# Optimization experiments

Measured on AMD Instinct MI355X. Metric: run time of the kernel, lower is better.

## Reference

```python
import jax, jax.numpy as jnp
import numpy as np

B = 8192      # sessions
L = 64        # tokens per session
T = B * L     # total tokens
H = 128       # hidden_size
MAX_LEN = 64  # position_emb has MAX_LEN+1 rows


def setup_inputs() -> dict:
    key = jax.random.key(0)
    ks = jax.random.split(key, 10)
    s1 = 1.0 / np.sqrt(H)
    s2 = 1.0 / np.sqrt(2 * H)
    hidden = jax.random.normal(ks[0], (T, H), jnp.float32)
    seq_len = jnp.full((B,), L, dtype=jnp.int32)
    # reversed positions 1..L within each session (<= MAX_LEN)
    reverse_pos = jnp.tile(jnp.arange(L, 0, -1, dtype=jnp.int32), B)
    return {
        "hidden": hidden,
        "pos_table": jax.random.normal(ks[1], (MAX_LEN + 1, H), jnp.float32) * 0.02,
        "W_pos_w": jax.random.normal(ks[2], (H, 2 * H), jnp.float32) * s2,
        "W_pos_b": jax.random.normal(ks[3], (H,), jnp.float32) * s2,
        "W1_w": jax.random.normal(ks[4], (H, H), jnp.float32) * s1,
        "W1_b": jax.random.normal(ks[5], (H,), jnp.float32) * s1,
        "W2_w": jax.random.normal(ks[6], (H, H), jnp.float32) * s1,
        "W2_b": jax.random.normal(ks[7], (H,), jnp.float32) * s1,
        "q_w": jax.random.normal(ks[8], (1, H), jnp.float32) * s1,
        "q_b": jax.random.normal(ks[9], (1,), jnp.float32) * s1,
        "seq_len": seq_len,
        "reverse_pos": reverse_pos,
    }


def reference(hidden, pos_table, W_pos_w, W_pos_b, W1_w, W1_b, W2_w, W2_b,
              q_w, q_b, seq_len, reverse_pos):
    Bn = seq_len.shape[0]
    Tn = hidden.shape[0]
    # token -> session id (replaces the python split loop)
    seg = jnp.repeat(jnp.arange(Bn), seq_len, total_repeat_length=Tn)  # [T]
    # per-session mean, broadcast back to tokens (v_mean_repeat_concat)
    mean = jax.ops.segment_sum(hidden, seg, num_segments=Bn) \
        / seq_len[:, None].astype(hidden.dtype)                        # [B,H]
    mean_rep = mean[seg]                                               # [T,H]
    pos_emb = pos_table[reverse_pos]                                   # [T,H]
    pos_hidden = jnp.tanh(
        jnp.concatenate([hidden, pos_emb], axis=-1) @ W_pos_w.T + W_pos_b
    )                                                                  # [T,H]
    gate = jax.nn.sigmoid(mean_rep @ W1_w.T + W1_b + pos_hidden @ W2_w.T + W2_b)
    alpha = gate @ q_w.T + q_b                                         # [T,1]
    # per-session sum of alpha-weighted tokens (h_s)
    return jax.ops.segment_sum(alpha * hidden, seg, num_segments=Bn)   # [B,H]
```

## Files before the change

kernel.cpp:

```cpp
#include <hip/hip_runtime.h>
#include <hip/hip_bf16.h>

typedef unsigned short u16;
typedef __bf16 bf16x8 __attribute__((ext_vector_type(8)));
typedef float  f32x4  __attribute__((ext_vector_type(4)));

__device__ __forceinline__ unsigned pk2(float a, float b) {
    __hip_bfloat162 h = __float22bfloat162_rn(make_float2(a, b));
    unsigned u; __builtin_memcpy(&u, &h, 4);
    return u;
}
__device__ __forceinline__ u16 f2b1(float f) { return (u16)(pk2(f, f) & 0xFFFFu); }

__device__ __forceinline__ bf16x8 pack8(const float4 a, const float4 b) {
    unsigned u0 = pk2(a.x, a.y), u1 = pk2(a.z, a.w);
    unsigned u2 = pk2(b.x, b.y), u3 = pk2(b.z, b.w);
    unsigned arr[4] = {u0, u1, u2, u3};
    bf16x8 r; __builtin_memcpy(&r, arr, 16);
    return r;
}

#define MFMA __builtin_amdgcn_mfma_f32_16x16x32_bf16

__global__ __launch_bounds__(128) void prep_kernel(
    const float* __restrict__ pos_table, const float* __restrict__ Wpw,
    const float* __restrict__ Wpb, const float* __restrict__ W2,
    const float* __restrict__ W1, const float* __restrict__ W1b,
    const float* __restrict__ W2b,
    float* __restrict__ ppK, u16* __restrict__ wb1, u16* __restrict__ wb2,
    u16* __restrict__ wb3, float* __restrict__ bsum)
{
    const int b = blockIdx.x, t = threadIdx.x;
    if (b < 65) {
        const float4* pr = (const float4*)(pos_table + b * 128);
        const float4* wr = (const float4*)(Wpw + t * 256 + 128);
        float acc = Wpb[t];
        #pragma unroll
        for (int k = 0; k < 32; ++k) {
            const float4 p = pr[k], wv = wr[k];
            acc += p.x * wv.x + p.y * wv.y + p.z * wv.z + p.w * wv.w;
        }
        ppK[b * 128 + t] = acc * 2.885390081777927f;
    } else {
        const int j = b - 65;
        const int off = (((j >> 4) * 4 + (t >> 5)) * 16 + (j & 15)) * 32 + (t & 31);
        wb1[off] = f2b1(Wpw[j * 256 + t]);
        wb2[off] = f2b1(W2[j * 128 + t]);
        wb3[off] = f2b1(W1[j * 128 + t]);
        if (j == 0) bsum[t] = W1b[t] + W2b[t];
    }
}

__global__ __launch_bounds__(256, 2) void fused_kernel(
    const float* __restrict__ hidden, const int* __restrict__ rpos,
    const float* __restrict__ qw, const float* __restrict__ qb,
    const float* __restrict__ ppK, const u16* __restrict__ wb1g,
    const u16* __restrict__ wb2g, const u16* __restrict__ wb3g,
    const float* __restrict__ bsum, float* __restrict__ out)
{
    __shared__ __align__(16) u16 phs[4 * 64 * 136];
    __shared__ __align__(16) float alphas[4 * 64];

    const int tid = threadIdx.x;
    const int w = tid >> 6;
    const int l = tid & 63;
    const int c = l & 15;
    const int g = l >> 4;
    const int s = blockIdx.x * 4 + w;
    const float* hs = hidden + (size_t)s * (64 * 128);
    u16* ph = phs + w * (64 * 136);
    float* alw = alphas + w * 64;

    bf16x8 af[4][4];
    float cs[4][8];
    #pragma unroll
    for (int kk = 0; kk < 4; ++kk)
        #pragma unroll
        for (int j = 0; j < 8; ++j) cs[kk][j] = 0.f;
    #pragma unroll
    for (int m = 0; m < 4; ++m)
        #pragma unroll
        for (int kk = 0; kk < 4; ++kk) {
            const float4* p = (const float4*)(hs + (16 * m + c) * 128 + 32 * kk + 8 * g);
            const float4 v0 = p[0], v1 = p[1];
            cs[kk][0] += v0.x; cs[kk][1] += v0.y; cs[kk][2] += v0.z; cs[kk][3] += v0.w;
            cs[kk][4] += v1.x; cs[kk][5] += v1.y; cs[kk][6] += v1.z; cs[kk][7] += v1.w;
            af[m][kk] = pack8(v0, v1);
        }

    #pragma unroll
    for (int msk = 1; msk <= 8; msk <<= 1)
        #pragma unroll
        for (int kk = 0; kk < 4; ++kk)
            #pragma unroll
            for (int j = 0; j < 8; ++j)
                cs[kk][j] += __shfl_xor(cs[kk][j], msk, 64);
    bf16x8 afm[4];
    #pragma unroll
    for (int kk = 0; kk < 4; ++kk) {
        float4 a, b;
        a.x = cs[kk][0] * (1.f / 64.f); a.y = cs[kk][1] * (1.f / 64.f);
        a.z = cs[kk][2] * (1.f / 64.f); a.w = cs[kk][3] * (1.f / 64.f);
        b.x = cs[kk][4] * (1.f / 64.f); b.y = cs[kk][5] * (1.f / 64.f);
        b.z = cs[kk][6] * (1.f / 64.f); b.w = cs[kk][7] * (1.f / 64.f);
        afm[kk] = pack8(a, b);
    }

    int pko[4][4];
    {
        const int* rp = rpos + s * 64;
        #pragma unroll
        for (int m = 0; m < 4; ++m) {
            const int4 rv = *(const int4*)(rp + 16 * m + 4 * g);
            pko[m][0] = rv.x * 128 + c; pko[m][1] = rv.y * 128 + c;
            pko[m][2] = rv.z * 128 + c; pko[m][3] = rv.w * 128 + c;
        }
    }

    {
        const u16* wb1p = wb1g + c * 32 + g * 8;
        const float K2 = 2.885390081777927f;
        #pragma unroll
        for (int n = 0; n < 8; ++n) {
            float ppv[4][4];
            #pragma unroll
            for (int m = 0; m < 4; ++m)
                #pragma unroll
                for (int r = 0; r < 4; ++r)
                    ppv[m][r] = ppK[pko[m][r] + 16 * n];
            const bf16x8 b0 = *(const bf16x8*)(wb1p + n * 2048);
            const bf16x8 b1 = *(const bf16x8*)(wb1p + n * 2048 + 512);
            const bf16x8 b2 = *(const bf16x8*)(wb1p + n * 2048 + 1024);
            const bf16x8 b3 = *(const bf16x8*)(wb1p + n * 2048 + 1536);
            f32x4 acc[4] = {};
            #pragma unroll
            for (int m = 0; m < 4; ++m) {
                acc[m] = MFMA(af[m][0], b0, acc[m], 0, 0, 0);
                acc[m] = MFMA(af[m][1], b1, acc[m], 0, 0, 0);
                acc[m] = MFMA(af[m][2], b2, acc[m], 0, 0, 0);
                acc[m] = MFMA(af[m][3], b3, acc[m], 0, 0, 0);
            }
            #pragma unroll
            for (int m = 0; m < 4; ++m)
                #pragma unroll
                for (int r = 0; r < 4; ++r) {
                    const float arg = fmaf(acc[m][r], K2, ppv[m][r]);
                    const float e2 = __builtin_amdgcn_exp2f(arg);
                    const float rc = __builtin_amdgcn_rcpf(e2 + 1.f);
                    ph[(16 * m + 4 * g + r) * 136 + 16 * n + c] =
                        f2b1(fmaf(-2.f, rc, 1.f));
                }
        }
    }

    bf16x8 af2[4][4];
    #pragma unroll
    for (int m = 0; m < 4; ++m)
        #pragma unroll
        for (int kk = 0; kk < 4; ++kk)
            af2[m][kk] = *(const bf16x8*)&ph[(16 * m + c) * 136 + kk * 32 + g * 8];

    {
        const u16* wb2p = wb2g + c * 32 + g * 8;
        const u16* wb3p = wb3g + c * 32 + g * 8;
        const float K1 = 1.4426950408889634f;
        float prt[4][4] = {};
        #pragma unroll
        for (int n = 0; n < 8; ++n) {
            const bf16x8 m0 = *(const bf16x8*)(wb3p + n * 2048);
            const bf16x8 m1 = *(const bf16x8*)(wb3p + n * 2048 + 512);
            const bf16x8 m2 = *(const bf16x8*)(wb3p + n * 2048 + 1024);
            const bf16x8 m3 = *(const bf16x8*)(wb3p + n * 2048 + 1536);
            f32x4 accM = {};
            accM = MFMA(afm[0], m0, accM, 0, 0, 0);
            accM = MFMA(afm[1], m1, accM, 0, 0, 0);
            accM = MFMA(afm[2], m2, accM, 0, 0, 0);
            accM = MFMA(afm[3], m3, accM, 0, 0, 0);
            const bf16x8 b0 = *(const bf16x8*)(wb2p + n * 2048);
            const bf16x8 b1 = *(const bf16x8*)(wb2p + n * 2048 + 512);
            const bf16x8 b2 = *(const bf16x8*)(wb2p + n * 2048 + 1024);
            const bf16x8 b3 = *(const bf16x8*)(wb2p + n * 2048 + 1536);
            const float gvn = -K1 * bsum[16 * n + c];
            const float qv  = qw[16 * n + c];
            #pragma unroll
            for (int m = 0; m < 4; ++m) {
                f32x4 a = accM;
                a = MFMA(af2[m][0], b0, a, 0, 0, 0);
                a = MFMA(af2[m][1], b1, a, 0, 0, 0);
                a = MFMA(af2[m][2], b2, a, 0, 0, 0);
                a = MFMA(af2[m][3], b3, a, 0, 0, 0);
                #pragma unroll
                for (int r = 0; r < 4; ++r) {
                    const float arg = fmaf(a[r], -K1, gvn);
                    const float e2 = __builtin_amdgcn_exp2f(arg);
                    const float rc = __builtin_amdgcn_rcpf(e2 + 1.f);
                    prt[m][r] = fmaf(rc, qv, prt[m][r]);
                }
            }
        }
        #pragma unroll
        for (int msk = 1; msk <= 8; msk <<= 1)
            #pragma unroll
            for (int m = 0; m < 4; ++m)
                #pragma unroll
                for (int r = 0; r < 4; ++r)
                    prt[m][r] += __shfl_xor(prt[m][r], msk, 64);
        if (c == 0) {
            const float qbv = qb[0];
            #pragma unroll
            for (int m = 0; m < 4; ++m)
                #pragma unroll
                for (int r = 0; r < 4; ++r)
                    alw[16 * m + 4 * g + r] = prt[m][r] + qbv;
        }
    }

    {
        float a0[4] = {0.f, 0.f, 0.f, 0.f}, a1[4] = {0.f, 0.f, 0.f, 0.f};
        #pragma unroll
        for (int t4 = 0; t4 < 16; ++t4) {
            const float4 av = *(const float4*)&alw[t4 * 4];
            const float* hr = hs + (t4 * 4) * 128;
            a0[0] = fmaf(av.x, hr[l], a0[0]);       a1[0] = fmaf(av.x, hr[64 + l], a1[0]);
            a0[1] = fmaf(av.y, hr[128 + l], a0[1]); a1[1] = fmaf(av.y, hr[192 + l], a1[1]);
            a0[2] = fmaf(av.z, hr[256 + l], a0[2]); a1[2] = fmaf(av.z, hr[320 + l], a1[2]);
            a0[3] = fmaf(av.w, hr[384 + l], a0[3]); a1[3] = fmaf(av.w, hr[448 + l], a1[3]);
        }
        out[(size_t)s * 128 + l]      = (a0[0] + a0[1]) + (a0[2] + a0[3]);
        out[(size_t)s * 128 + 64 + l] = (a1[0] + a1[1]) + (a1[2] + a1[3]);
    }
}

extern "C" void kernel_launch(void* const* d_in, const int* in_sizes, int n_in,
                              void* d_out, int out_size, void* d_ws, size_t ws_size,
                              hipStream_t stream)
{
    const float* hidden    = (const float*)d_in[0];
    const float* pos_table = (const float*)d_in[1];
    const float* Wpw       = (const float*)d_in[2];
    const float* Wpb       = (const float*)d_in[3];
    const float* W1w       = (const float*)d_in[4];
    const float* W1b       = (const float*)d_in[5];
    const float* W2w       = (const float*)d_in[6];
    const float* W2b       = (const float*)d_in[7];
    const float* qw        = (const float*)d_in[8];
    const float* qb        = (const float*)d_in[9];
    const int*   rpos      = (const int*)d_in[11];
    float* out = (float*)d_out;

    const int B = in_sizes[10];

    char* wsb = (char*)d_ws;
    float* ppK  = (float*)wsb;
    u16*   wb1  = (u16*)(wsb + 33280);
    u16*   wb2  = (u16*)(wsb + 33280 + 32768);
    u16*   wb3  = (u16*)(wsb + 33280 + 2 * 32768);
    float* bsum = (float*)(wsb + 33280 + 3 * 32768);

    prep_kernel<<<193, 128, 0, stream>>>(pos_table, Wpw, Wpb, W2w, W1w, W1b, W2b,
                                         ppK, wb1, wb2, wb3, bsum);
    fused_kernel<<<B / 4, 256, 0, stream>>>(hidden, rpos, qw, qb,
                                            ppK, wb1, wb2, wb3, bsum, out);
}
```

Measured before the change: 437.9 us.

## Split each session across two waves to cut registers and raise occupancy

Each session's 64 tokens are now handled by two waves of 32 tokens each. The per-session mean is combined through shared memory behind a block barrier, and the final weighted sum is likewise split across the two waves. This halves per-wave register arrays and shared memory, and launch bounds now target 4 blocks per CU so more waves can hide memory latency. In exchange it adds two __syncthreads, extra shared-memory traffic, and reloads the W2 and W1 weight fragments per wave, doubling weight-load work per token.

```diff
diff --git a/kernel.cpp b/kernel.cpp
--- a/kernel.cpp
+++ b/kernel.cpp
@@ -51,38 +51,41 @@
     }
 }
 
-__global__ __launch_bounds__(256, 2) void fused_kernel(
+__global__ __launch_bounds__(256, 4) void fused_kernel(
     const float* __restrict__ hidden, const int* __restrict__ rpos,
     const float* __restrict__ qw, const float* __restrict__ qb,
     const float* __restrict__ ppK, const u16* __restrict__ wb1g,
     const u16* __restrict__ wb2g, const u16* __restrict__ wb3g,
     const float* __restrict__ bsum, float* __restrict__ out)
 {
-    __shared__ __align__(16) u16 phs[4 * 64 * 136];
-    __shared__ __align__(16) float alphas[4 * 64];
+    __shared__ __align__(16) u16 phs[4 * 32 * 136];
+    __shared__ __align__(16) float meanv[4 * 128];
+    __shared__ __align__(16) float alphas[2 * 64];
 
     const int tid = threadIdx.x;
     const int w = tid >> 6;
     const int l = tid & 63;
     const int c = l & 15;
     const int g = l >> 4;
-    const int s = blockIdx.x * 4 + w;
+    const int sl = w >> 1;
+    const int p  = w & 1;
+    const int s  = blockIdx.x * 2 + sl;
     const float* hs = hidden + (size_t)s * (64 * 128);
-    u16* ph = phs + w * (64 * 136);
-    float* alw = alphas + w * 64;
-
-    bf16x8 af[4][4];
+    const float* hw = hs + p * (32 * 128);
+    u16* ph = phs + w * (32 * 136);
+
+    bf16x8 af[2][4];
     float cs[4][8];
     #pragma unroll
     for (int kk = 0; kk < 4; ++kk)
         #pragma unroll
         for (int j = 0; j < 8; ++j) cs[kk][j] = 0.f;
     #pragma unroll
-    for (int m = 0; m < 4; ++m)
+    for (int m = 0; m < 2; ++m)
         #pragma unroll
         for (int kk = 0; kk < 4; ++kk) {
-            const float4* p = (const float4*)(hs + (16 * m + c) * 128 + 32 * kk + 8 * g);
-            const float4 v0 = p[0], v1 = p[1];
+            const float4* ptr = (const float4*)(hw + (16 * m + c) * 128 + 32 * kk + 8 * g);
+            const float4 v0 = ptr[0], v1 = ptr[1];
             cs[kk][0] += v0.x; cs[kk][1] += v0.y; cs[kk][2] += v0.z; cs[kk][3] += v0.w;
             cs[kk][4] += v1.x; cs[kk][5] += v1.y; cs[kk][6] += v1.z; cs[kk][7] += v1.w;
             af[m][kk] = pack8(v0, v1);
@@ -95,36 +98,54 @@
             #pragma unroll
             for (int j = 0; j < 8; ++j)
                 cs[kk][j] += __shfl_xor(cs[kk][j], msk, 64);
-    bf16x8 afm[4];
-    #pragma unroll
-    for (int kk = 0; kk < 4; ++kk) {
-        float4 a, b;
-        a.x = cs[kk][0] * (1.f / 64.f); a.y = cs[kk][1] * (1.f / 64.f);
-        a.z = cs[kk][2] * (1.f / 64.f); a.w = cs[kk][3] * (1.f / 64.f);
-        b.x = cs[kk][4] * (1.f / 64.f); b.y = cs[kk][5] * (1.f / 64.f);
-        b.z = cs[kk][6] * (1.f / 64.f); b.w = cs[kk][7] * (1.f / 64.f);
-        afm[kk] = pack8(a, b);
-    }
-
-    int pko[4][4];
-    {
-        const int* rp = rpos + s * 64;
-        #pragma unroll
-        for (int m = 0; m < 4; ++m) {
+    if (c < 8) {
+        const int kk = c >> 1, j0 = (c & 1) * 4;
+        float4 v;
+        v.x = cs[kk][j0];     v.y = cs[kk][j0 + 1];
+        v.z = cs[kk][j0 + 2]; v.w = cs[kk][j0 + 3];
+        *(float4*)&meanv[(sl * 2 + p) * 128 + 32 * kk + 8 * g + j0] = v;
+    }
+
+    int pko[2][4];
+    {
+        const int* rp = rpos + s * 64 + p * 32;
+        #pragma unroll
+        for (int m = 0; m < 2; ++m) {
             const int4 rv = *(const int4*)(rp + 16 * m + 4 * g);
             pko[m][0] = rv.x * 128 + c; pko[m][1] = rv.y * 128 + c;
             pko[m][2] = rv.z * 128 + c; pko[m][3] = rv.w * 128 + c;
         }
     }
 
+    __syncthreads();
+
+    bf16x8 afm[4];
+    {
+        const float* mv0 = meanv + (sl * 2 + 0) * 128;
+        const float* mv1 = meanv + (sl * 2 + 1) * 128;
+        #pragma unroll
+        for (int kk = 0; kk < 4; ++kk) {
+            const float4 a0 = *(const float4*)&mv0[32 * kk + 8 * g];
+            const float4 a1 = *(const float4*)&mv1[32 * kk + 8 * g];
+            const float4 b0 = *(const float4*)&mv0[32 * kk + 8 * g + 4];
+            const float4 b1 = *(const float4*)&mv1[32 * kk + 8 * g + 4];
+            float4 a, b;
+            a.x = (a0.x + a1.x) * (1.f / 64.f); a.y = (a0.y + a1.y) * (1.f / 64.f);
+            a.z = (a0.z + a1.z) * (1.f / 64.f); a.w = (a0.w + a1.w) * (1.f / 64.f);
+            b.x = (b0.x + b1.x) * (1.f / 64.f); b.y = (b0.y + b1.y) * (1.f / 64.f);
+            b.z = (b0.z + b1.z) * (1.f / 64.f); b.w = (b0.w + b1.w) * (1.f / 64.f);
+            afm[kk] = pack8(a, b);
+        }
+    }
+
     {
         const u16* wb1p = wb1g + c * 32 + g * 8;
         const float K2 = 2.885390081777927f;
         #pragma unroll
         for (int n = 0; n < 8; ++n) {
-            float ppv[4][4];
-            #pragma unroll
-            for (int m = 0; m < 4; ++m)
+            float ppv[2][4];
+            #pragma unroll
+            for (int m = 0; m < 2; ++m)
                 #pragma unroll
                 for (int r = 0; r < 4; ++r)
                     ppv[m][r] = ppK[pko[m][r] + 16 * n];
@@ -132,16 +153,16 @@
             const bf16x8 b1 = *(const bf16x8*)(wb1p + n * 2048 + 512);
             const bf16x8 b2 = *(const bf16x8*)(wb1p + n * 2048 + 1024);
             const bf16x8 b3 = *(const bf16x8*)(wb1p + n * 2048 + 1536);
-            f32x4 acc[4] = {};
-            #pragma unroll
-            for (int m = 0; m < 4; ++m) {
+            f32x4 acc[2] = {};
+            #pragma unroll
+            for (int m = 0; m < 2; ++m) {
                 acc[m] = MFMA(af[m][0], b0, acc[m], 0, 0, 0);
                 acc[m] = MFMA(af[m][1], b1, acc[m], 0, 0, 0);
                 acc[m] = MFMA(af[m][2], b2, acc[m], 0, 0, 0);
                 acc[m] = MFMA(af[m][3], b3, acc[m], 0, 0, 0);
             }
             #pragma unroll
-            for (int m = 0; m < 4; ++m)
+            for (int m = 0; m < 2; ++m)
                 #pragma unroll
                 for (int r = 0; r < 4; ++r) {
                     const float arg = fmaf(acc[m][r], K2, ppv[m][r]);
@@ -153,9 +174,9 @@
         }
     }
 
-    bf16x8 af2[4][4];
-    #pragma unroll
-    for (int m = 0; m < 4; ++m)
+    bf16x8 af2[2][4];
+    #pragma unroll
+    for (int m = 0; m < 2; ++m)
         #pragma unroll
         for (int kk = 0; kk < 4; ++kk)
             af2[m][kk] = *(const bf16x8*)&ph[(16 * m + c) * 136 + kk * 32 + g * 8];
@@ -164,7 +185,7 @@
         const u16* wb2p = wb2g + c * 32 + g * 8;
         const u16* wb3p = wb3g + c * 32 + g * 8;
         const float K1 = 1.4426950408889634f;
-        float prt[4][4] = {};
+        float prt[2][4] = {};
         #pragma unroll
         for (int n = 0; n < 8; ++n) {
             const bf16x8 m0 = *(const bf16x8*)(wb3p + n * 2048);
@@ -183,7 +204,7 @@
             const float gvn = -K1 * bsum[16 * n + c];
             const float qv  = qw[16 * n + c];
             #pragma unroll
-            for (int m = 0; m < 4; ++m) {
+            for (int m = 0; m < 2; ++m) {
                 f32x4 a = accM;
                 a = MFMA(af2[m][0], b0, a, 0, 0, 0);
                 a = MFMA(af2[m][1], b1, a, 0, 0, 0);
@@ -201,33 +222,35 @@
         #pragma unroll
         for (int msk = 1; msk <= 8; msk <<= 1)
             #pragma unroll
-            for (int m = 0; m < 4; ++m)
+            for (int m = 0; m < 2; ++m)
                 #pragma unroll
                 for (int r = 0; r < 4; ++r)
                     prt[m][r] += __shfl_xor(prt[m][r], msk, 64);
         if (c == 0) {
             const float qbv = qb[0];
             #pragma unroll
-            for (int m = 0; m < 4; ++m)
+            for (int m = 0; m < 2; ++m)
                 #pragma unroll
                 for (int r = 0; r < 4; ++r)
-                    alw[16 * m + 4 * g + r] = prt[m][r] + qbv;
-        }
-    }
-
-    {
-        float a0[4] = {0.f, 0.f, 0.f, 0.f}, a1[4] = {0.f, 0.f, 0.f, 0.f};
+                    alphas[sl * 64 + p * 32 + 16 * m + 4 * g + r] = prt[m][r] + qbv;
+        }
+    }
+    __syncthreads();
+
+    {
+        const int h = p * 64 + l;
+        const float* alw = alphas + sl * 64;
+        float a0 = 0.f, a1 = 0.f, a2 = 0.f, a3 = 0.f;
         #pragma unroll
         for (int t4 = 0; t4 < 16; ++t4) {
             const float4 av = *(const float4*)&alw[t4 * 4];
-            const float* hr = hs + (t4 * 4) * 128;
-            a0[0] = fmaf(av.x, hr[l], a0[0]);       a1[0] = fmaf(av.x, hr[64 + l], a1[0]);
-            a0[1] = fmaf(av.y, hr[128 + l], a0[1]); a1[1] = fmaf(av.y, hr[192 + l], a1[1]);
-            a0[2] = fmaf(av.z, hr[256 + l], a0[2]); a1[2] = fmaf(av.z, hr[320 + l], a1[2]);
-            a0[3] = fmaf(av.w, hr[384 + l], a0[3]); a1[3] = fmaf(av.w, hr[448 + l], a1[3]);
-        }
-        out[(size_t)s * 128 + l]      = (a0[0] + a0[1]) + (a0[2] + a0[3]);
-        out[(size_t)s * 128 + 64 + l] = (a1[0] + a1[1]) + (a1[2] + a1[3]);
+            const float* hr = hs + (t4 * 4) * 128 + h;
+            a0 = fmaf(av.x, hr[0],   a0);
+            a1 = fmaf(av.y, hr[128], a1);
+            a2 = fmaf(av.z, hr[256], a2);
+            a3 = fmaf(av.w, hr[384], a3);
+        }
+        out[(size_t)s * 128 + h] = (a0 + a1) + (a2 + a3);
     }
 }
 
@@ -259,6 +282,6 @@
 
     prep_kernel<<<193, 128, 0, stream>>>(pos_table, Wpw, Wpb, W2w, W1w, W1b, W2b,
                                          ppK, wb1, wb2, wb3, bsum);
-    fused_kernel<<<B / 4, 256, 0, stream>>>(hidden, rpos, qw, qb,
+    fused_kernel<<<B / 2, 256, 0, stream>>>(hidden, rpos, qw, qb,
                                             ppK, wb1, wb2, wb3, bsum, out);
 }
```

Result: slower. 507.4 us (+15.9%).
